# Performance work log

Hardware: AMD Instinct MI355X
Metric: run time of the kernel (lower is better)

## Reference

```python
import jax, jax.numpy as jnp
import numpy as np

B, S, E, R = 64, 2048, 256, 50


def setup_inputs() -> dict:
    key = jax.random.key(0)
    ks = jax.random.split(key, 22)
    n = lambda k, shp, s=0.05: (jax.random.normal(k, shp, jnp.float32) * s)
    d = {
        "encoder_o": jax.random.normal(ks[0], (B, S, E), jnp.float32),
        "h0": jax.random.normal(ks[1], (1, B, E), jnp.float32),
        "c0": jax.random.normal(ks[2], (1, B, E), jnp.float32),
        "r_in": jax.random.randint(ks[3], (B,), 0, R),
        "k1": jax.random.randint(ks[4], (B, 1), 0, S),
        "k2": jax.random.randint(ks[5], (B, 1), 0, S),
        "W_ih": n(ks[6], (4 * E, E)),
        "W_hh": n(ks[7], (4 * E, E)),
        "b_ih": n(ks[8], (4 * E,)),
        "b_hh": n(ks[9], (4 * E,)),
        "W_attn": n(ks[10], (E, 2 * E)),
        "b_attn": n(ks[11], (E,)),
        "W_conv": n(ks[12], (E, 2 * E, 3)),
        "b_conv": n(ks[13], (E,)),
        "sos_emb": n(ks[14], (1, E)),
        "rel_emb": n(ks[15], (R, E)),
        "W_rel": n(ks[16], (R, E)),
        "b_rel": n(ks[17], (R,)),
        "W_ent1": n(ks[18], (1, E)),
        "b_ent1": n(ks[19], (1,)),
        "W_ent2": n(ks[20], (1, E)),
        "b_ent2": n(ks[21], (1,)),
    }
    return d


def reference(encoder_o, h0, c0, r_in, k1, k2, W_ih, W_hh, b_ih, b_hh,
              W_attn, b_attn, W_conv, b_conv, sos_emb, rel_emb,
              W_rel, b_rel, W_ent1, b_ent1, W_ent2, b_ent2):
    Bx, Sx, Ex = encoder_o.shape

    def lstm_step(x, h, c):  # single decode step, x/h/c: [B,E]
        gates = x @ W_ih.T + h @ W_hh.T + (b_ih + b_hh)  # [B,4E]
        i, f, g, o = jnp.split(gates, 4, axis=-1)        # PyTorch gate order i,f,g,o
        c2 = jax.nn.sigmoid(f) * c + jax.nn.sigmoid(i) * jnp.tanh(g)
        h2 = jax.nn.sigmoid(o) * jnp.tanh(c2)
        return h2, c2

    def attend(q):  # Luong dot attention + tanh(linear(cat(mix,q))); q: [B,E]
        scores = jnp.einsum('be,bse->bs', q, encoder_o)
        attn = jax.nn.softmax(scores, axis=-1)
        mix = jnp.einsum('bs,bse->be', attn, encoder_o)
        comb = jnp.concatenate([mix, q], axis=-1)        # [B,2E]
        return jnp.tanh(comb @ W_attn.T + b_attn)

    def step(x, h, c):
        h2, c2 = lstm_step(x, h, c)
        return attend(h2), h2, c2

    kern = jnp.transpose(W_conv, (2, 1, 0))  # [3, 2E, E] for NWC/WIO

    def ent_heads(o):  # o: [B,E]
        vec = jnp.broadcast_to(o[:, None, :], (Bx, Sx, Ex))  # seq_and_vec
        feat = jnp.concatenate([encoder_o, vec], axis=-1)    # [B,S,2E]
        conv = jax.lax.conv_general_dilated(
            feat, kern, (1,), 'SAME',
            dimension_numbers=('NWC', 'WIO', 'NWC')) + b_conv
        conv = jax.nn.relu(conv)                             # [B,S,E]
        e1 = conv @ W_ent1.T + b_ent1                        # [B,S,1]
        e2 = conv @ W_ent2.T + b_ent2
        return e1, e2

    h, c = h0[0], c0[0]
    # t1: <sos> -> relation logits
    x = jnp.broadcast_to(sos_emb[0], (Bx, Ex))
    out1, h, c = step(x, h, c)
    t1_out = out1 @ W_rel.T + b_rel                          # [B,R]
    # t2: relation embedding -> entity-1 span heads
    out2, h, c = step(rel_emb[r_in], h, c)
    e1a, e2a = ent_heads(out2)
    # t3: gathered k1+k2 encoder vectors -> entity-2 span heads
    idx = jnp.arange(Bx)
    kk = encoder_o[idx, k1[:, 0]] + encoder_o[idx, k2[:, 0]]  # vectorized seq_gather
    out3, h, c = step(kk, h, c)
    e1b, e2b = ent_heads(out3)
    # pack outputs: [B, R + 4*S]
    return jnp.concatenate(
        [t1_out, e1a[..., 0], e2a[..., 0], e1b[..., 0], e2b[..., 0]], axis=1)
```

## Files before the change

kernel.cpp:

```cpp
#include <hip/hip_runtime.h>
#include <hip/hip_bf16.h>

#define EE 256
#define SS 2048
#define BB 64
#define RN 50
#define OSTR 8242

typedef __attribute__((ext_vector_type(4))) float vf4;
typedef __attribute__((ext_vector_type(8))) short s8v;
typedef __attribute__((ext_vector_type(4))) short s4v;
typedef __attribute__((ext_vector_type(4))) unsigned short u16x4;
typedef __attribute__((ext_vector_type(2))) unsigned int u32x2;

__device__ __forceinline__ unsigned short f2bf(float f){
  __hip_bfloat16 h = __float2bfloat16(f);
  return *reinterpret_cast<unsigned short*>(&h);
}
__device__ __forceinline__ unsigned int f2bf2(float a, float b){
  __hip_bfloat162 h = __float22bfloat162_rn(make_float2(a, b));
  return *reinterpret_cast<unsigned int*>(&h);
}
__device__ __forceinline__ float sigm(float x){ return 1.0f/(1.0f + __expf(-x)); }
__device__ __forceinline__ float dot4(vf4 a, vf4 b){ return a.x*b.x + a.y*b.y + a.z*b.z + a.w*b.w; }

__device__ __forceinline__ vf4 mfma16(s4v a, s4v b, vf4 c){
#if __has_builtin(__builtin_amdgcn_mfma_f32_16x16x16bf16_1k)
  return __builtin_amdgcn_mfma_f32_16x16x16bf16_1k(a, b, c, 0, 0, 0);
#else
  vf4 d;
  asm volatile("v_mfma_f32_16x16x16_bf16 %0, %1, %2, %3\n\ts_nop 7\n\ts_nop 7"
               : "=v"(d) : "v"(a), "v"(b), "v"(c));
  return d;
#endif
}

__device__ __forceinline__ void gload_lds16(const void* g, void* l){
  __builtin_amdgcn_global_load_lds(
      (const __attribute__((address_space(1))) unsigned int*)g,
      (__attribute__((address_space(3))) unsigned int*)l, 16, 0, 0);
}

__global__ __launch_bounds__(256) void k_prep(
  const float* __restrict__ enc, const float* __restrict__ h0, const float* __restrict__ c0,
  const int* __restrict__ r_in, const int* __restrict__ k1, const int* __restrict__ k2,
  const float* __restrict__ sos, const float* __restrict__ rel,
  const float* __restrict__ W_conv,
  float* __restrict__ xT, float* __restrict__ hT0, float* __restrict__ cT,
  unsigned short* __restrict__ WT, unsigned short* __restrict__ Bp)
{
  int bid = blockIdx.x, t = threadIdx.x;
  if (bid < 256){
    int part = bid >> 6, b = bid & 63;
    if (part == 0){
      xT[(size_t)0*EE*BB + t*BB + b] = sos[t];
    } else if (part == 1){
      xT[(size_t)1*EE*BB + t*BB + b] = rel[r_in[b]*EE + t];
    } else if (part == 2){
      int i1 = k1[b], i2 = k2[b];
      xT[(size_t)2*EE*BB + t*BB + b] =
        enc[((size_t)b*SS + i1)*EE + t] + enc[((size_t)b*SS + i2)*EE + t];
    } else {
      hT0[t*BB + b] = h0[b*EE + t];
      cT [t*BB + b] = c0[b*EE + t];
    }
  } else if (bid < 512){
    int o = bid - 256;
    for (int r = t; r < 768; r += 256)
      WT[(size_t)r*EE + o] = f2bf(W_conv[(size_t)o*1536 + 768 + r]);
  } else {
    int gid = (bid - 512)*256 + t;
    int kc  = gid >> 10;
    int rem = gid & 1023;
    int ni  = rem >> 6;
    int l   = rem & 63;
    int o   = ni*16 + (l & 15);
    int kbase = kc*32 + ((l >> 4) << 3);
    u16x4 lo4, hi4;
    #pragma unroll
    for (int j=0;j<8;++j){
      int k = kbase + j; int ktap = k >> 8; int i = k & 255;
      unsigned short v = f2bf(W_conv[((size_t)o*512 + i)*3 + ktap]);
      if (j<4){ if(j==0)lo4.x=v; else if(j==1)lo4.y=v; else if(j==2)lo4.z=v; else lo4.w=v; }
      else    { if(j==4)hi4.x=v; else if(j==5)hi4.y=v; else if(j==6)hi4.z=v; else hi4.w=v; }
    }
    u16x4* dst = (u16x4*)(Bp + (size_t)gid*8);
    dst[0] = lo4; dst[1] = hi4;
  }
}

__global__ __launch_bounds__(256) void k_step(
  const float* __restrict__ hT_cur, const float* __restrict__ xT_st,
  const float* __restrict__ W_ih, const float* __restrict__ W_hh,
  const float* __restrict__ b_ih, const float* __restrict__ b_hh,
  float* __restrict__ cT, float* __restrict__ hT_next, float* __restrict__ hs_st)
{
  int e = blockIdx.x, tid = threadIdx.x;
  int w = tid >> 6, b = tid & 63;
  int grow = w*EE + e;
  const float* wh = W_hh + (size_t)grow*EE;
  const float* wi = W_ih + (size_t)grow*EE;
  float acc = b_ih[grow] + b_hh[grow];
  #pragma unroll 4
  for (int k4 = 0; k4 < EE/4; ++k4){
    vf4 wh4 = *(const vf4*)(wh + k4*4);
    vf4 wi4 = *(const vf4*)(wi + k4*4);
    int k = k4*4;
    acc += hT_cur[(k+0)*BB+b]*wh4.x + hT_cur[(k+1)*BB+b]*wh4.y
         + hT_cur[(k+2)*BB+b]*wh4.z + hT_cur[(k+3)*BB+b]*wh4.w;
    acc += xT_st[(k+0)*BB+b]*wi4.x + xT_st[(k+1)*BB+b]*wi4.y
         + xT_st[(k+2)*BB+b]*wi4.z + xT_st[(k+3)*BB+b]*wi4.w;
  }
  __shared__ float sm[4][BB];
  sm[w][b] = acc;
  __syncthreads();
  if (tid < BB){
    float iv = sm[0][tid], fv = sm[1][tid], gv = sm[2][tid], ov = sm[3][tid];
    float cprev = cT[e*BB + tid];
    float cn = sigm(fv)*cprev + sigm(iv)*tanhf(gv);
    float hn = sigm(ov)*tanhf(cn);
    cT[e*BB + tid] = cn;
    hT_next[e*BB + tid] = hn;
    hs_st[(size_t)tid*EE + e] = hn;
  }
}

__global__ __launch_bounds__(256) void k_attend(
  const float* __restrict__ enc, const float* __restrict__ hs,
  float* __restrict__ mixc, float* __restrict__ stats,
  unsigned short* __restrict__ encb)
{
  int bid = blockIdx.x; int b = bid >> 3, ch = bid & 7;
  int tid = threadIdx.x, lane = tid & 63, wv = tid >> 6;
  __shared__ float hsm[3][EE];
  __shared__ float wgt[3][256];
  __shared__ float red[3][4];
  __shared__ float mg[3];
  __shared__ vf4 mpart[4][3][64];
  for (int i = tid; i < 3*EE; i += 256) hsm[i>>8][i&255] = hs[((size_t)(i>>8)*BB + b)*EE + (i&255)];
  __syncthreads();
  int s = ch*256 + tid;
  const vf4* er = (const vf4*)(enc + ((size_t)b*SS + s)*EE);
  const vf4* q0 = (const vf4*)hsm[0];
  const vf4* q1 = (const vf4*)hsm[1];
  const vf4* q2 = (const vf4*)hsm[2];
  float a0=0.f, a1=0.f, a2=0.f;
  #pragma unroll 8
  for (int k = 0; k < EE/4; ++k){
    vf4 ev = er[k];
    a0 += dot4(ev, q0[k]);
    a1 += dot4(ev, q1[k]);
    a2 += dot4(ev, q2[k]);
  }
  float m0=a0, m1=a1, m2=a2;
  #pragma unroll
  for (int d=1; d<64; d<<=1){
    m0 = fmaxf(m0, __shfl_xor(m0,d));
    m1 = fmaxf(m1, __shfl_xor(m1,d));
    m2 = fmaxf(m2, __shfl_xor(m2,d));
  }
  if (lane==0){ red[0][wv]=m0; red[1][wv]=m1; red[2][wv]=m2; }
  __syncthreads();
  if (tid < 3) mg[tid] = fmaxf(fmaxf(red[tid][0],red[tid][1]), fmaxf(red[tid][2],red[tid][3]));
  __syncthreads();
  float e0 = __expf(a0-mg[0]), e1 = __expf(a1-mg[1]), e2 = __expf(a2-mg[2]);
  wgt[0][tid]=e0; wgt[1][tid]=e1; wgt[2][tid]=e2;
  #pragma unroll
  for (int d=1; d<64; d<<=1){
    e0 += __shfl_xor(e0,d); e1 += __shfl_xor(e1,d); e2 += __shfl_xor(e2,d);
  }
  if (lane==0){ red[0][wv]=e0; red[1][wv]=e1; red[2][wv]=e2; }
  __syncthreads();
  if (tid < 3){
    float l = red[tid][0]+red[tid][1]+red[tid][2]+red[tid][3];
    int o = ((tid*BB + b)*8 + ch)*2;
    stats[o] = mg[tid]; stats[o+1] = l;
  }
  __syncthreads();
  vf4 A0 = (vf4)0.0f, A1 = (vf4)0.0f, A2 = (vf4)0.0f;
  for (int i=0;i<64;++i){
    int sl = wv*64 + i;
    int gs = ch*256 + sl;
    vf4 ev = *(const vf4*)(enc + ((size_t)b*SS + gs)*EE + lane*4);
    if (encb){
      u32x2 pk; pk.x = f2bf2(ev.x, ev.y); pk.y = f2bf2(ev.z, ev.w);
      int off = (lane*8) ^ (((gs + 1) & 7) << 4);
      *(u32x2*)((char*)encb + ((size_t)b*SS + gs)*512 + off) = pk;
    }
    A0 += ev*wgt[0][sl]; A1 += ev*wgt[1][sl]; A2 += ev*wgt[2][sl];
  }
  mpart[wv][0][lane]=A0; mpart[wv][1][lane]=A1; mpart[wv][2][lane]=A2;
  __syncthreads();
  if (tid < 192){
    int q = tid >> 6, e4 = tid & 63;
    vf4 sum = mpart[0][q][e4] + mpart[1][q][e4] + mpart[2][q][e4] + mpart[3][q][e4];
    *(vf4*)(mixc + ((size_t)(q*BB+b)*8 + ch)*EE + e4*4) = sum;
  }
}

__global__ __launch_bounds__(256) void k_post(
  const float* __restrict__ mixc, const float* __restrict__ hs,
  const float* __restrict__ stats,
  const float* __restrict__ W_attn, const float* __restrict__ b_attn,
  const float* __restrict__ W_rel, const float* __restrict__ b_rel,
  const unsigned short* __restrict__ WT, const float* __restrict__ b_conv,
  float* __restrict__ out, float* __restrict__ vv)
{
  int b = blockIdx.x, t = threadIdx.x;
  __shared__ float comb[3][2*EE];
  __shared__ float o1[EE], o2s[EE], o3s[EE];
  #pragma unroll
  for (int q=0;q<3;q++){
    float M = -1e30f;
    #pragma unroll
    for (int c=0;c<8;c++) M = fmaxf(M, stats[((q*BB+b)*8 + c)*2]);
    float L = 0.f;
    float scl[8];
    #pragma unroll
    for (int c=0;c<8;c++){
      int o = ((q*BB+b)*8 + c)*2;
      float e = __expf(stats[o]-M);
      scl[c] = e; L += stats[o+1]*e;
    }
    float invL = 1.0f/L;
    float m = 0.f;
    #pragma unroll
    for (int c=0;c<8;c++) m += mixc[((size_t)(q*BB+b)*8 + c)*EE + t] * scl[c];
    comb[q][t] = m * invL;
    comb[q][EE+t] = hs[((size_t)q*BB + b)*EE + t];
  }
  __syncthreads();
  float a0 = b_attn[t], a1 = a0, a2 = a0;
  const vf4* wr = (const vf4*)(W_attn + (size_t)t*2*EE);
  const vf4* c0v = (const vf4*)comb[0];
  const vf4* c1v = (const vf4*)comb[1];
  const vf4* c2v = (const vf4*)comb[2];
  #pragma unroll 4
  for (int k=0;k<2*EE/4;++k){
    vf4 w = wr[k];
    a0 += dot4(w, c0v[k]); a1 += dot4(w, c1v[k]); a2 += dot4(w, c2v[k]);
  }
  o1[t]=tanhf(a0); o2s[t]=tanhf(a1); o3s[t]=tanhf(a2);
  __syncthreads();
  if (t < RN){
    float acc = b_rel[t];
    const vf4* wrel = (const vf4*)(W_rel + (size_t)t*EE);
    const vf4* ov = (const vf4*)o1;
    for (int k=0;k<EE/4;++k) acc += dot4(wrel[k], ov[k]);
    out[(size_t)b*OSTR + t] = acc;
  }
  float va0=0,va1=0,va2=0, vb0=0,vb1=0,vb2=0;
  for (int i=0;i<EE;++i){
    float x2 = o2s[i], x3 = o3s[i];
    const unsigned short* wt = WT + (size_t)i*3*EE + t;
    float w0 = __uint_as_float(((unsigned int)wt[0]) << 16);
    float w1 = __uint_as_float(((unsigned int)wt[EE]) << 16);
    float w2 = __uint_as_float(((unsigned int)wt[2*EE]) << 16);
    va0 += x2*w0; va1 += x2*w1; va2 += x2*w2;
    vb0 += x3*w0; vb1 += x3*w1; vb2 += x3*w2;
  }
  float bc = b_conv[t];
  vv[((0*3+0)*BB + b)*EE + t] = va0+va1+va2+bc;
  vv[((0*3+1)*BB + b)*EE + t] = va1+va2+bc;
  vv[((0*3+2)*BB + b)*EE + t] = va0+va1+bc;
  vv[((1*3+0)*BB + b)*EE + t] = vb0+vb1+vb2+bc;
  vv[((1*3+1)*BB + b)*EE + t] = vb1+vb2+bc;
  vv[((1*3+2)*BB + b)*EE + t] = vb0+vb1+bc;
}

__global__ __launch_bounds__(256, 3) void k_conv(
  const float* __restrict__ enc, const unsigned short* __restrict__ encb,
  const unsigned short* __restrict__ Bp,
  const float* __restrict__ vv,
  const float* __restrict__ W_e1, const float* __restrict__ b_e1,
  const float* __restrict__ W_e2, const float* __restrict__ b_e2,
  float* __restrict__ out)
{
  int stile = blockIdx.x, b = blockIdx.y;
  int s0 = stile*64;
  int tid = threadIdx.x, lane = tid & 63, w = tid >> 6;
  int lo = lane & 15, hi = lane >> 4;
  __shared__ __align__(16) unsigned short Ab[66*256];
  __shared__ float part2[4][64][4];

  if (encb){
    const char* ebase = (const char*)encb + (size_t)b*SS*512;
    for (int base = 0; base < 66*32; base += 256){
      int idx = base + tid;
      if (idx < 66*32){
        int r = idx >> 5, c = idx & 31;
        int srow = s0 - 1 + r;
        srow = srow < 0 ? 0 : (srow > SS-1 ? SS-1 : srow);
        gload_lds16(ebase + (size_t)srow*512 + c*16, (char*)Ab + idx*16);
      }
    }
    __syncthreads();
    if (stile == 0 || stile == 31){
      if (stile == 0  && tid < 32) *(vf4*)((char*)Ab + tid*16) = (vf4)0.0f;
      if (stile == 31 && tid < 32) *(vf4*)((char*)Ab + 65*512 + tid*16) = (vf4)0.0f;
      __syncthreads();
    }
  } else {
    const float* eb = enc + (size_t)b*SS*EE;
    for (int idx = tid; idx < 66*64; idx += 256){
      int r = idx >> 6, c4 = idx & 63;
      int s = s0 - 1 + r;
      vf4 v = (vf4)0.0f;
      if (s >= 0 && s < SS) v = *(const vf4*)(eb + (size_t)s*EE + c4*4);
      u32x2 pk; pk.x = f2bf2(v.x, v.y); pk.y = f2bf2(v.z, v.w);
      int byte = (r*512 + c4*8) ^ ((r & 7) << 4);
      *(u32x2*)((char*)Ab + byte) = pk;
    }
    __syncthreads();
  }

  vf4 acc[4][4];
  #pragma unroll
  for (int oi=0;oi<4;++oi){
    #pragma unroll
    for (int si=0;si<4;++si) acc[oi][si] = (vf4)0.0f;
  }
  const s8v* Bp8 = (const s8v*)Bp;
  s8v bf[4], bfn[4];
  #pragma unroll
  for (int oi=0;oi<4;++oi) bf[oi] = Bp8[((0*16 + (w*4+oi)) << 6) + lane];

  for (int kc=0; kc<24; ++kc){
    int ktap = kc >> 3;
    int colb = ((kc & 7) << 6) + (hi << 4);
    s8v af[4];
    #pragma unroll
    for (int si=0;si<4;++si){
      int row = si*16 + lo + ktap;
      int byte = row*512 + (colb ^ ((row & 7) << 4));
      af[si] = *(const s8v*)((const char*)Ab + byte);
    }
    if (kc < 23){
      #pragma unroll
      for (int oi=0;oi<4;++oi) bfn[oi] = Bp8[(((kc+1)*16 + (w*4+oi)) << 6) + lane];
    }
    #pragma unroll
    for (int oi=0;oi<4;++oi){
      #pragma unroll
      for (int si=0;si<4;++si)
        acc[oi][si] = __builtin_amdgcn_mfma_f32_16x16x32_bf16(bf[oi], af[si], acc[oi][si], 0, 0, 0);
    }
    #pragma unroll
    for (int oi=0;oi<4;++oi) bf[oi] = bfn[oi];
  }

  bool firstTile = (s0 == 0), lastTile = (s0 + 64 == SS);
  vf4 vaI[4], vbI[4]; s4v aw[4];
  #pragma unroll
  for (int oi=0;oi<4;++oi){
    int o4 = w*64 + oi*16 + hi*4;
    vaI[oi] = *(const vf4*)(vv + ((0*3+0)*BB + b)*EE + o4);
    vbI[oi] = *(const vf4*)(vv + ((1*3+0)*BB + b)*EE + o4);
    vf4 w1 = *(const vf4*)(W_e1 + o4);
    vf4 w2 = *(const vf4*)(W_e2 + o4);
    float e0 = (lo==0) ? w1.x : ((lo==1) ? w2.x : 0.0f);
    float e1 = (lo==0) ? w1.y : ((lo==1) ? w2.y : 0.0f);
    float e2 = (lo==0) ? w1.z : ((lo==1) ? w2.z : 0.0f);
    float e3 = (lo==0) ? w1.w : ((lo==1) ? w2.w : 0.0f);
    u32x2 t; t.x = f2bf2(e0, e1); t.y = f2bf2(e2, e3);
    aw[oi] = __builtin_bit_cast(s4v, t);
  }
  #pragma unroll
  for (int si=0; si<4; ++si){
    vf4 Da = (vf4)0.0f, Db = (vf4)0.0f;
    #pragma unroll
    for (int oi=0; oi<4; ++oi){
      int o4 = w*64 + oi*16 + hi*4;
      vf4 c = acc[oi][si];
      vf4 va = vaI[oi], vb = vbI[oi];
      if (firstTile && si==0 && lo==0){
        va = *(const vf4*)(vv + ((0*3+1)*BB + b)*EE + o4);
        vb = *(const vf4*)(vv + ((1*3+1)*BB + b)*EE + o4);
      }
      if (lastTile && si==3 && lo==15){
        va = *(const vf4*)(vv + ((0*3+2)*BB + b)*EE + o4);
        vb = *(const vf4*)(vv + ((1*3+2)*BB + b)*EE + o4);
      }
      float a0 = fmaxf(c.x+va.x,0.f), a1 = fmaxf(c.y+va.y,0.f);
      float a2 = fmaxf(c.z+va.z,0.f), a3 = fmaxf(c.w+va.w,0.f);
      float b0 = fmaxf(c.x+vb.x,0.f), b1 = fmaxf(c.y+vb.y,0.f);
      float b2 = fmaxf(c.z+vb.z,0.f), b3 = fmaxf(c.w+vb.w,0.f);
      u32x2 ta; ta.x = f2bf2(a0,a1); ta.y = f2bf2(a2,a3);
      u32x2 tb; tb.x = f2bf2(b0,b1); tb.y = f2bf2(b2,b3);
      Da = mfma16(aw[oi], __builtin_bit_cast(s4v, ta), Da);
      Db = mfma16(aw[oi], __builtin_bit_cast(s4v, tb), Db);
    }
    if (hi == 0){
      vf4 pk; pk.x = Da.x; pk.y = Da.y; pk.z = Db.x; pk.w = Db.y;
      *(vf4*)&part2[w][si*16+lo][0] = pk;
    }
  }
  __syncthreads();
  {
    int s = tid >> 2, c = tid & 3;
    float r = part2[0][s][c] + part2[1][s][c] + part2[2][s][c] + part2[3][s][c];
    r += (c & 1) ? b_e2[0] : b_e1[0];
    out[(size_t)b*OSTR + RN + c*SS + (s0 + s)] = r;
  }
}

extern "C" void kernel_launch(void* const* d_in, const int* in_sizes, int n_in,
                              void* d_out, int out_size, void* d_ws, size_t ws_size,
                              hipStream_t stream)
{
  const float* enc   = (const float*)d_in[0];
  const float* h0    = (const float*)d_in[1];
  const float* c0    = (const float*)d_in[2];
  const int*   r_in  = (const int*)d_in[3];
  const int*   k1    = (const int*)d_in[4];
  const int*   k2    = (const int*)d_in[5];
  const float* W_ih  = (const float*)d_in[6];
  const float* W_hh  = (const float*)d_in[7];
  const float* b_ih  = (const float*)d_in[8];
  const float* b_hh  = (const float*)d_in[9];
  const float* W_attn= (const float*)d_in[10];
  const float* b_attn= (const float*)d_in[11];
  const float* W_conv= (const float*)d_in[12];
  const float* b_conv= (const float*)d_in[13];
  const float* sos   = (const float*)d_in[14];
  const float* rel   = (const float*)d_in[15];
  const float* W_rel = (const float*)d_in[16];
  const float* b_rel = (const float*)d_in[17];
  const float* W_e1  = (const float*)d_in[18];
  const float* b_e1  = (const float*)d_in[19];
  const float* W_e2  = (const float*)d_in[20];
  const float* b_e2  = (const float*)d_in[21];
  float* out = (float*)d_out;
  char* ws = (char*)d_ws;

  float* hs    = (float*)(ws);
  float* vv    = (float*)(ws + 196608);
  float* stats = (float*)(ws + 589824);
  float* mixc  = (float*)(ws + 602112);
  unsigned short* Bp = (unsigned short*)(ws + 2174976);
  float* xT    = (float*)(ws + 2568192);
  float* hTa   = (float*)(ws + 2764800);
  float* hTb   = (float*)(ws + 2830336);
  float* cT    = (float*)(ws + 2895872);
  unsigned short* WT = (unsigned short*)(ws + 2961408);
  size_t encb_off = 3354624;
  size_t need = encb_off + (size_t)BB*SS*EE*2;
  unsigned short* encb = (ws_size >= need) ? (unsigned short*)(ws + encb_off) : nullptr;

  hipLaunchKernelGGL(k_prep,  dim3(608), dim3(256), 0, stream,
                     enc,h0,c0,r_in,k1,k2,sos,rel,W_conv, xT,hTa,cT, WT,Bp);
  hipLaunchKernelGGL(k_step,  dim3(256), dim3(256), 0, stream,
                     hTa, xT + 0*EE*BB, W_ih,W_hh,b_ih,b_hh, cT, hTb, hs + 0*BB*EE);
  hipLaunchKernelGGL(k_step,  dim3(256), dim3(256), 0, stream,
                     hTb, xT + 1*EE*BB, W_ih,W_hh,b_ih,b_hh, cT, hTa, hs + 1*BB*EE);
  hipLaunchKernelGGL(k_step,  dim3(256), dim3(256), 0, stream,
                     hTa, xT + 2*EE*BB, W_ih,W_hh,b_ih,b_hh, cT, hTb, hs + 2*BB*EE);
  hipLaunchKernelGGL(k_attend,dim3(512), dim3(256), 0, stream, enc, hs, mixc, stats, encb);
  hipLaunchKernelGGL(k_post,  dim3(64),  dim3(256), 0, stream,
                     mixc, hs, stats, W_attn,b_attn, W_rel,b_rel, WT, b_conv, out, vv);
  hipLaunchKernelGGL(k_conv,  dim3(32,64), dim3(256), 0, stream,
                     enc, encb, Bp, vv, W_e1,b_e1, W_e2,b_e2, out);
}
```

Before: 217.5 us.

## Stage encoder rows in LDS and split attention into 32 chunks per batch

The attention kernel now copies each 64-row chunk of the encoder into shared memory with direct global-to-LDS loads. It then reuses that copy for both the score dot products and the weighted mix, so the encoder is read from global memory once instead of twice. The grid grows from 512 to 2048 blocks (32 chunks per batch) for more parallelism, and the bf16 copy of the encoder is written with 16-byte stores. In exchange, the post kernel has to merge 32 partial softmax stats and mix vectors instead of 8, and each block uses about 80KB of LDS, which limits occupancy.

```diff
diff --git a/kernel.cpp b/kernel.cpp
--- a/kernel.cpp
+++ b/kernel.cpp
@@ -6,12 +6,14 @@
 #define BB 64
 #define RN 50
 #define OSTR 8242
+#define NCH 32
 
 typedef __attribute__((ext_vector_type(4))) float vf4;
 typedef __attribute__((ext_vector_type(8))) short s8v;
 typedef __attribute__((ext_vector_type(4))) short s4v;
 typedef __attribute__((ext_vector_type(4))) unsigned short u16x4;
 typedef __attribute__((ext_vector_type(2))) unsigned int u32x2;
+typedef __attribute__((ext_vector_type(4))) unsigned int u32x4;
 
 __device__ __forceinline__ unsigned short f2bf(float f){
   __hip_bfloat16 h = __float2bfloat16(f);
@@ -125,76 +127,101 @@
   }
 }
 
-__global__ __launch_bounds__(256) void k_attend(
+__global__ __launch_bounds__(256, 2) void k_attend(
   const float* __restrict__ enc, const float* __restrict__ hs,
   float* __restrict__ mixc, float* __restrict__ stats,
   unsigned short* __restrict__ encb)
 {
-  int bid = blockIdx.x; int b = bid >> 3, ch = bid & 7;
+  int bid = blockIdx.x; int b = bid >> 5, ch = bid & 31;
   int tid = threadIdx.x, lane = tid & 63, wv = tid >> 6;
-  __shared__ float hsm[3][EE];
-  __shared__ float wgt[3][256];
-  __shared__ float red[3][4];
-  __shared__ float mg[3];
-  __shared__ vf4 mpart[4][3][64];
-  for (int i = tid; i < 3*EE; i += 256) hsm[i>>8][i&255] = hs[((size_t)(i>>8)*BB + b)*EE + (i&255)];
-  __syncthreads();
-  int s = ch*256 + tid;
-  const vf4* er = (const vf4*)(enc + ((size_t)b*SS + s)*EE);
-  const vf4* q0 = (const vf4*)hsm[0];
-  const vf4* q1 = (const vf4*)hsm[1];
-  const vf4* q2 = (const vf4*)hsm[2];
-  float a0=0.f, a1=0.f, a2=0.f;
-  #pragma unroll 8
-  for (int k = 0; k < EE/4; ++k){
-    vf4 ev = er[k];
-    a0 += dot4(ev, q0[k]);
-    a1 += dot4(ev, q1[k]);
-    a2 += dot4(ev, q2[k]);
-  }
-  float m0=a0, m1=a1, m2=a2;
-  #pragma unroll
-  for (int d=1; d<64; d<<=1){
-    m0 = fmaxf(m0, __shfl_xor(m0,d));
-    m1 = fmaxf(m1, __shfl_xor(m1,d));
-    m2 = fmaxf(m2, __shfl_xor(m2,d));
-  }
-  if (lane==0){ red[0][wv]=m0; red[1][wv]=m1; red[2][wv]=m2; }
-  __syncthreads();
-  if (tid < 3) mg[tid] = fmaxf(fmaxf(red[tid][0],red[tid][1]), fmaxf(red[tid][2],red[tid][3]));
-  __syncthreads();
-  float e0 = __expf(a0-mg[0]), e1 = __expf(a1-mg[1]), e2 = __expf(a2-mg[2]);
-  wgt[0][tid]=e0; wgt[1][tid]=e1; wgt[2][tid]=e2;
-  #pragma unroll
-  for (int d=1; d<64; d<<=1){
-    e0 += __shfl_xor(e0,d); e1 += __shfl_xor(e1,d); e2 += __shfl_xor(e2,d);
-  }
-  if (lane==0){ red[0][wv]=e0; red[1][wv]=e1; red[2][wv]=e2; }
-  __syncthreads();
-  if (tid < 3){
-    float l = red[tid][0]+red[tid][1]+red[tid][2]+red[tid][3];
-    int o = ((tid*BB + b)*8 + ch)*2;
-    stats[o] = mg[tid]; stats[o+1] = l;
-  }
-  __syncthreads();
-  vf4 A0 = (vf4)0.0f, A1 = (vf4)0.0f, A2 = (vf4)0.0f;
-  for (int i=0;i<64;++i){
-    int sl = wv*64 + i;
-    int gs = ch*256 + sl;
-    vf4 ev = *(const vf4*)(enc + ((size_t)b*SS + gs)*EE + lane*4);
-    if (encb){
-      u32x2 pk; pk.x = f2bf2(ev.x, ev.y); pk.y = f2bf2(ev.z, ev.w);
-      int off = (lane*8) ^ (((gs + 1) & 7) << 4);
-      *(u32x2*)((char*)encb + ((size_t)b*SS + gs)*512 + off) = pk;
-    }
-    A0 += ev*wgt[0][sl]; A1 += ev*wgt[1][sl]; A2 += ev*wgt[2][sl];
-  }
-  mpart[wv][0][lane]=A0; mpart[wv][1][lane]=A1; mpart[wv][2][lane]=A2;
+  __shared__ __align__(16) float rows[64*260];
+  __shared__ float sc[3][64];
+  __shared__ __align__(16) char smx[12288];
+  float* hsm = (float*)smx;
+  vf4 (*mpart)[3][64] = (vf4(*)[3][64])smx;
+
+  const float* rowbase = enc + ((size_t)b*SS + ch*64)*EE;
+  #pragma unroll
+  for (int j=0;j<16;++j){
+    int r = wv*16 + j;
+    gload_lds16(rowbase + (size_t)r*EE + lane*4, (char*)rows + r*1040);
+  }
+  for (int i = tid; i < 3*EE; i += 256)
+    hsm[i] = hs[((size_t)(i>>8)*BB + b)*EE + (i&255)];
+  __syncthreads();
+
+  {
+    int r = tid >> 2, q = tid & 3;
+    const vf4* rp = (const vf4*)(rows + r*260 + q*64);
+    const vf4* q0 = (const vf4*)(hsm + 0*EE + q*64);
+    const vf4* q1 = (const vf4*)(hsm + 1*EE + q*64);
+    const vf4* q2 = (const vf4*)(hsm + 2*EE + q*64);
+    int gs = ch*64 + r;
+    char* ebase = encb ? ((char*)encb + ((size_t)b*SS + gs)*512 + q*128) : nullptr;
+    int key = ((gs + 1) & 7) << 4;
+    float a0=0.f, a1=0.f, a2=0.f;
+    u32x2 prev;
+    #pragma unroll
+    for (int k=0;k<16;++k){
+      vf4 ev = rp[k];
+      a0 += dot4(ev, q0[k]);
+      a1 += dot4(ev, q1[k]);
+      a2 += dot4(ev, q2[k]);
+      if (ebase){
+        u32x2 pk; pk.x = f2bf2(ev.x, ev.y); pk.y = f2bf2(ev.z, ev.w);
+        if (k & 1){
+          u32x4 st4; st4.x = prev.x; st4.y = prev.y; st4.z = pk.x; st4.w = pk.y;
+          *(u32x4*)(ebase + (((k>>1)*16) ^ key)) = st4;
+        } else prev = pk;
+      }
+    }
+    a0 += __shfl_xor(a0,1); a0 += __shfl_xor(a0,2);
+    a1 += __shfl_xor(a1,1); a1 += __shfl_xor(a1,2);
+    a2 += __shfl_xor(a2,1); a2 += __shfl_xor(a2,2);
+    if (q == 0){ sc[0][r] = a0; sc[1][r] = a1; sc[2][r] = a2; }
+  }
+  __syncthreads();
+
+  if (tid < 64){
+    float s0 = sc[0][tid], s1 = sc[1][tid], s2 = sc[2][tid];
+    float m0=s0, m1=s1, m2=s2;
+    #pragma unroll
+    for (int d=1; d<64; d<<=1){
+      m0 = fmaxf(m0, __shfl_xor(m0,d));
+      m1 = fmaxf(m1, __shfl_xor(m1,d));
+      m2 = fmaxf(m2, __shfl_xor(m2,d));
+    }
+    float e0 = __expf(s0-m0), e1 = __expf(s1-m1), e2 = __expf(s2-m2);
+    sc[0][tid]=e0; sc[1][tid]=e1; sc[2][tid]=e2;
+    float l0=e0, l1=e1, l2=e2;
+    #pragma unroll
+    for (int d=1; d<64; d<<=1){
+      l0 += __shfl_xor(l0,d); l1 += __shfl_xor(l1,d); l2 += __shfl_xor(l2,d);
+    }
+    if (tid == 0){
+      int o0 = ((0*BB+b)*NCH + ch)*2; stats[o0]=m0; stats[o0+1]=l0;
+      int o1 = ((1*BB+b)*NCH + ch)*2; stats[o1]=m1; stats[o1+1]=l1;
+      int o2 = ((2*BB+b)*NCH + ch)*2; stats[o2]=m2; stats[o2+1]=l2;
+    }
+  }
+  __syncthreads();
+
+  {
+    vf4 A0 = (vf4)0.0f, A1 = (vf4)0.0f, A2 = (vf4)0.0f;
+    #pragma unroll 4
+    for (int j=0;j<16;++j){
+      int r = wv*16 + j;
+      float w0 = sc[0][r], w1 = sc[1][r], w2 = sc[2][r];
+      vf4 ev = *(const vf4*)(rows + r*260 + lane*4);
+      A0 += ev*w0; A1 += ev*w1; A2 += ev*w2;
+    }
+    mpart[wv][0][lane]=A0; mpart[wv][1][lane]=A1; mpart[wv][2][lane]=A2;
+  }
   __syncthreads();
   if (tid < 192){
     int q = tid >> 6, e4 = tid & 63;
     vf4 sum = mpart[0][q][e4] + mpart[1][q][e4] + mpart[2][q][e4] + mpart[3][q][e4];
-    *(vf4*)(mixc + ((size_t)(q*BB+b)*8 + ch)*EE + e4*4) = sum;
+    *(vf4*)(mixc + ((size_t)(q*BB+b)*NCH + ch)*EE + e4*4) = sum;
   }
 }
 
@@ -212,21 +239,15 @@
   #pragma unroll
   for (int q=0;q<3;q++){
     float M = -1e30f;
-    #pragma unroll
-    for (int c=0;c<8;c++) M = fmaxf(M, stats[((q*BB+b)*8 + c)*2]);
-    float L = 0.f;
-    float scl[8];
-    #pragma unroll
-    for (int c=0;c<8;c++){
-      int o = ((q*BB+b)*8 + c)*2;
+    for (int c=0;c<NCH;c++) M = fmaxf(M, stats[((q*BB+b)*NCH + c)*2]);
+    float L = 0.f, macc = 0.f;
+    for (int c=0;c<NCH;c++){
+      int o = ((q*BB+b)*NCH + c)*2;
       float e = __expf(stats[o]-M);
-      scl[c] = e; L += stats[o+1]*e;
-    }
-    float invL = 1.0f/L;
-    float m = 0.f;
-    #pragma unroll
-    for (int c=0;c<8;c++) m += mixc[((size_t)(q*BB+b)*8 + c)*EE + t] * scl[c];
-    comb[q][t] = m * invL;
+      L += stats[o+1]*e;
+      macc += mixc[((size_t)(q*BB+b)*NCH + c)*EE + t] * e;
+    }
+    comb[q][t] = macc / L;
     comb[q][EE+t] = hs[((size_t)q*BB + b)*EE + t];
   }
   __syncthreads();
@@ -436,14 +457,14 @@
   float* hs    = (float*)(ws);
   float* vv    = (float*)(ws + 196608);
   float* stats = (float*)(ws + 589824);
-  float* mixc  = (float*)(ws + 602112);
-  unsigned short* Bp = (unsigned short*)(ws + 2174976);
-  float* xT    = (float*)(ws + 2568192);
-  float* hTa   = (float*)(ws + 2764800);
-  float* hTb   = (float*)(ws + 2830336);
-  float* cT    = (float*)(ws + 2895872);
-  unsigned short* WT = (unsigned short*)(ws + 2961408);
-  size_t encb_off = 3354624;
+  float* mixc  = (float*)(ws + 638976);
+  unsigned short* Bp = (unsigned short*)(ws + 6930432);
+  float* xT    = (float*)(ws + 7323648);
+  float* hTa   = (float*)(ws + 7520256);
+  float* hTb   = (float*)(ws + 7585792);
+  float* cT    = (float*)(ws + 7651328);
+  unsigned short* WT = (unsigned short*)(ws + 7716864);
+  size_t encb_off = 8110080;
   size_t need = encb_off + (size_t)BB*SS*EE*2;
   unsigned short* encb = (ws_size >= need) ? (unsigned short*)(ws + encb_off) : nullptr;
 
@@ -455,7 +476,7 @@
                      hTb, xT + 1*EE*BB, W_ih,W_hh,b_ih,b_hh, cT, hTa, hs + 1*BB*EE);
   hipLaunchKernelGGL(k_step,  dim3(256), dim3(256), 0, stream,
                      hTa, xT + 2*EE*BB, W_ih,W_hh,b_ih,b_hh, cT, hTb, hs + 2*BB*EE);
-  hipLaunchKernelGGL(k_attend,dim3(512), dim3(256), 0, stream, enc, hs, mixc, stats, encb);
+  hipLaunchKernelGGL(k_attend,dim3(2048), dim3(256), 0, stream, enc, hs, mixc, stats, encb);
   hipLaunchKernelGGL(k_post,  dim3(64),  dim3(256), 0, stream,
                      mixc, hs, stats, W_attn,b_attn, W_rel,b_rel, WT, b_conv, out, vv);
   hipLaunchKernelGGL(k_conv,  dim3(32,64), dim3(256), 0, stream,
```

Measured after the change: 216.6 us. About the same (-0.4%).
